# Kernel optimization log

Measured on AMD Instinct MI355X. Metric: run time of the kernel, lower is better.

The kernel has to match this reference:

```python
import jax, jax.numpy as jnp
import numpy as np

B, T, XD, H, ZD, L = 1024, 100, 38, 500, 16, 3


def _gru(x, Wih, Whh, bih, bhh):
    # torch nn.GRU (batch_first), gate order r,z,n. x: [B,T,D] -> [B,T,H]
    Hh = Whh.shape[1]
    xW = jnp.einsum('btd,gd->btg', x, Wih) + bih  # precompute input proj [B,T,3H]
    def step(h, xw_t):
        hW = h @ Whh.T + bhh
        r = jax.nn.sigmoid(xw_t[:, :Hh] + hW[:, :Hh])
        zg = jax.nn.sigmoid(xw_t[:, Hh:2 * Hh] + hW[:, Hh:2 * Hh])
        n = jnp.tanh(xw_t[:, 2 * Hh:] + r * hW[:, 2 * Hh:])
        h_new = (1.0 - zg) * n + zg * h
        return h_new, h_new
    h0 = jnp.zeros((x.shape[0], Hh), x.dtype)
    _, hs = jax.lax.scan(step, h0, jnp.swapaxes(xW, 0, 1))
    return jnp.swapaxes(hs, 0, 1)


def _u_hat(u, w):
    # invertibility-constrained u for planar flow
    wu = jnp.dot(w, u)
    m = -1.0 + jax.nn.softplus(wu)
    return u + (m - wu) * w / (jnp.sum(w * w) + 1e-6)


def setup_inputs() -> dict:
    key = jax.random.key(0)
    ks = jax.random.split(key, 24)
    def lin_init(k, shape, fan_in):
        bound = 1.0 / np.sqrt(fan_in)
        return jax.random.uniform(k, shape, jnp.float32, -bound, bound)
    inp = {}
    inp['x'] = jax.random.normal(ks[0], (B, T, XD), jnp.float32)
    inp['eps'] = jax.random.normal(ks[1], (B, T, ZD), jnp.float32)
    # q_rnn GRU
    inp['Wih_q'] = lin_init(ks[2], (3 * H, XD), H)
    inp['Whh_q'] = lin_init(ks[3], (3 * H, H), H)
    inp['bih_q'] = lin_init(ks[4], (3 * H,), H)
    inp['bhh_q'] = lin_init(ks[5], (3 * H,), H)
    # q_mean / q_std linears on [h_t, z_prev]
    inp['Wqm'] = lin_init(ks[6], (ZD, H + ZD), H + ZD)
    inp['bqm'] = lin_init(ks[7], (ZD,), H + ZD)
    inp['Wqs'] = lin_init(ks[8], (ZD, H + ZD), H + ZD)
    inp['bqs'] = lin_init(ks[9], (ZD,), H + ZD)
    # p_rnn GRU
    inp['Wih_p'] = lin_init(ks[10], (3 * H, ZD), H)
    inp['Whh_p'] = lin_init(ks[11], (3 * H, H), H)
    inp['bih_p'] = lin_init(ks[12], (3 * H,), H)
    inp['bhh_p'] = lin_init(ks[13], (3 * H,), H)
    # p_mean / p_std linears
    inp['Wpm'] = lin_init(ks[14], (XD, H), H)
    inp['bpm'] = lin_init(ks[15], (XD,), H)
    inp['Wps'] = lin_init(ks[16], (XD, H), H)
    inp['bps'] = lin_init(ks[17], (XD,), H)
    # planar flow params (torch.randn init)
    inp['fu'] = jax.random.normal(ks[18], (L, ZD), jnp.float32)
    inp['fw'] = jax.random.normal(ks[19], (L, ZD), jnp.float32)
    inp['fb'] = jax.random.normal(ks[20], (L,), jnp.float32)
    return inp


def reference(x, eps, Wih_q, Whh_q, bih_q, bhh_q, Wqm, bqm, Wqs, bqs,
              Wih_p, Whh_p, bih_p, bhh_p, Wpm, bpm, Wps, bps, fu, fw, fb):
    q_out = _gru(x, Wih_q, Whh_q, bih_q, bhh_q)  # [B,T,H]
    u_hats = jax.vmap(_u_hat)(fu, fw)            # [L,ZD], data-independent

    def step(carry, inp_t):
        z_prev, ld_sum = carry
        h_t, eps_t = inp_t
        comb = jnp.concatenate([h_t, z_prev], axis=1)          # [B,H+ZD]
        mu = comb @ Wqm.T + bqm
        std = jax.nn.softplus(comb @ Wqs.T + bqs) + 1e-4
        zk = mu + eps_t * std
        for k in range(L):  # small fixed number of flows
            w = fw[k]; uh = u_hats[k]
            hh = jnp.tanh(zk @ w + fb[k])[:, None]             # [B,1]
            zk = zk + uh[None, :] * hh
            psi = (1.0 - hh * hh) * w[None, :]                 # [B,ZD]
            det = 1.0 + psi @ uh                               # [B]
            ld_sum = ld_sum + jnp.log(jnp.abs(det) + 1e-6)[:, None]
        return (zk, ld_sum), (zk, mu, std)

    z0 = jnp.zeros((x.shape[0], ZD), x.dtype)
    ld0 = jnp.zeros((x.shape[0], 1), x.dtype)
    (_, log_det_sum), (z_seq, z0_mu, z0_std) = jax.lax.scan(
        step, (z0, ld0), (jnp.swapaxes(q_out, 0, 1), jnp.swapaxes(eps, 0, 1)))
    z_seq = jnp.swapaxes(z_seq, 0, 1)
    z0_mu = jnp.swapaxes(z0_mu, 0, 1)
    z0_std = jnp.swapaxes(z0_std, 0, 1)

    p_out = _gru(z_seq, Wih_p, Whh_p, bih_p, bhh_p)            # [B,T,H]
    recon_mu = p_out @ Wpm.T + bpm
    recon_std = jax.nn.softplus(p_out @ Wps.T + bps) + 1e-4
    return recon_mu, recon_std, z_seq, z0_mu, z0_std, log_det_sum
```

## Files before the change

### kernel.cpp

```cpp
#include <hip/hip_runtime.h>
#include <cmath>


#define B_  1024
#define T_  100
#define XD_ 38
#define H_  500
#define ZD_ 16
#define L_  3
#define NPHASE (T_ + 3)

typedef short bf16x8 __attribute__((ext_vector_type(8)));
typedef float f32x4  __attribute__((ext_vector_type(4)));
typedef unsigned short ushort;

#define HS ((size_t)B_ * 512)
#define ZS ((size_t)B_ * 32)

#define MFMA16(a, b, c) __builtin_amdgcn_mfma_f32_16x16x32_bf16((a), (b), (c), 0, 0, 0)

static __device__ __forceinline__ ushort f2bf(float f) {
    union { float f; unsigned u; } v; v.f = f;
    return (ushort)((v.u + 0x7FFF + ((v.u >> 16) & 1)) >> 16);
}
static __device__ __forceinline__ float sigf(float x) { return 1.0f / (1.0f + __expf(-x)); }
static __device__ __forceinline__ float tanh_(float x) {
    float e = __expf(2.0f * x);
    return 1.0f - 2.0f / (e + 1.0f);
}
static __device__ __forceinline__ float softplus_(float x) {
    return fmaxf(x, 0.0f) + log1pf(__expf(-fabsf(x)));
}
static __device__ __forceinline__ float grp16_sum(float v) {
    v += __shfl_xor(v, 1, 16);
    v += __shfl_xor(v, 2, 16);
    v += __shfl_xor(v, 4, 16);
    v += __shfl_xor(v, 8, 16);
    return v;
}

static __device__ __forceinline__ unsigned aload(const unsigned* p) {
    return __hip_atomic_load(p, __ATOMIC_RELAXED, __HIP_MEMORY_SCOPE_AGENT);
}
static __device__ __forceinline__ void astore(unsigned* p, unsigned v) {
    __hip_atomic_store(p, v, __ATOMIC_RELAXED, __HIP_MEMORY_SCOPE_AGENT);
}

struct OmniArgs {
    const float *x, *eps;
    const float *Wih_q, *Whh_q, *bih_q, *bhh_q;
    const float *Wqm, *bqm, *Wqs, *bqs;
    const float *Wih_p, *Whh_p, *bih_p, *bhh_p;
    const float *Wpm, *bpm, *Wps, *bps;
    const float *fu, *fw, *fb;
    ushort *hqbf, *hpbf, *zbf, *Wqg, *Wpg;
    unsigned *bar;
    float *o_rm, *o_rs, *o_z, *o_zm, *o_zs, *o_ld;
};

static __device__ __forceinline__ void arrive(unsigned* slots, int slot,
                                              unsigned tgt, int tid) {
    asm volatile("s_waitcnt vmcnt(0)" ::: "memory");
    __syncthreads();
    if (tid == 0) astore(slots + slot * 32, tgt);
}
static __device__ __forceinline__ void waitall(unsigned* slots, unsigned tgt,
                                               int tid) {
    if (tid < 64) {
        const unsigned* sp = slots + (tid & 31) * 32;
        for (;;) {
            bool ok = aload(sp) >= tgt;
            if (__all(ok)) break;
            __builtin_amdgcn_s_sleep(1);
        }
    }
    __syncthreads();
    asm volatile("buffer_inv" ::: "memory");
}

__global__ __launch_bounds__(512)
void omni_persist(OmniArgs A)
{
    __shared__ ushort lds[55296] __attribute__((aligned(16)));
    __shared__ int sh_gc[2];

    const int tid = threadIdx.x;

    if (tid == 0) {
        unsigned xcd;
        asm volatile("s_getreg_b32 %0, hwreg(HW_REG_XCC_ID)" : "=s"(xcd));
        xcd &= 7u;
        unsigned s = __hip_atomic_fetch_add(A.bar + xcd * 2048 + 1152, 1u,
                                            __ATOMIC_RELAXED, __HIP_MEMORY_SCOPE_AGENT);
        sh_gc[0] = (int)xcd;
        sh_gc[1] = (int)(s & 31u);
    }
    __syncthreads();
    const int grp = sh_gc[0];
    const int qc  = sh_gc[1];
    unsigned* slots = A.bar + grp * 2048;

    const bool isRC = (qc < 5);
    const bool isFL = (qc >= 24);
    const int  flowIdx = qc - 24;
    const int  fw2 = flowIdx >> 1;
    const int  fmt = flowIdx & 1;
    const int  m0 = grp * 128;

    const int gtid = tid & 255;
    const bool isQg = (tid < 256);
    const int w2   = gtid >> 6;
    const int lane = tid & 63;
    const int ln   = lane & 15, qd = lane >> 4;

    const bool fwave = isQg && isFL && (w2 == fw2);

    ushort* Whl = lds + (isQg ? 0 : 24960);
    ushort* Wil = lds + (isQg ? 49920 : 53376);

    ushort* WqgG = A.Wqg + (size_t)grp * (32 * 544);
    ushort* WpgG = A.Wpg + (size_t)grp * (128 * 512);

    const int rA0 = m0 + w2*32 + ln;
    const int rA1 = rA0 + 16;
    const int rAf = fmt ? rA1 : rA0;

    {
        const float* WhhSrc = isQg ? A.Whh_q : A.Whh_p;
        for (int idx = gtid; idx < 3*16*512; idx += 256) {
            int k = idx & 511, n = (idx >> 9) & 15, g = idx >> 13;
            int col = qc*16 + n;
            float v = (k < H_ && col < H_) ? WhhSrc[(size_t)(g*H_ + col)*H_ + k] : 0.f;
            Whl[(g*16 + n)*520 + k] = f2bf(v);
        }
        if (isQg) {
            for (int idx = gtid; idx < 3*16*64; idx += 256) {
                int k = idx & 63, n = (idx >> 6) & 15, g = idx >> 10;
                int col = qc*16 + n;
                float v = (k < XD_ && col < H_) ? A.Wih_q[(size_t)(g*H_+col)*XD_ + k] : 0.f;
                Wil[(g*16 + n)*72 + k] = f2bf(v);
            }
            if (qc == 31) {
                for (int idx = gtid; idx < 32*544; idx += 256) {
                    int n = idx / 544, k = idx - n*544;
                    const float* src = (n < 16) ? (A.Wqm + n*(H_+ZD_))
                                                : (A.Wqs + (n-16)*(H_+ZD_));
                    float v = 0.f;
                    if (k < H_) v = src[k];
                    else if (k >= 512 && k < 512 + ZD_) v = src[H_ + (k - 512)];
                    WqgG[idx] = f2bf(v);
                }
            }
        } else {
            for (int idx = gtid; idx < 3*16*32; idx += 256) {
                int k = idx & 31, n = (idx >> 5) & 15, g = idx >> 9;
                int col = qc*16 + n;
                float v = (k < ZD_ && col < H_) ? A.Wih_p[(size_t)(g*H_+col)*ZD_ + k] : 0.f;
                Wil[(g*16 + n)*40 + k] = f2bf(v);
            }
            if (isRC) {
                for (int idx = gtid; idx < 16*512; idx += 256) {
                    int k = idx & 511, n = idx >> 9;
                    int col = qc*16 + n;
                    float v = 0.f;
                    if (k < H_) {
                        if (col < XD_)        v = A.Wpm[(size_t)col*H_ + k];
                        else if (col < 2*XD_) v = A.Wps[(size_t)(col - XD_)*H_ + k];
                    }
                    WpgG[(size_t)(qc*16 + n)*512 + k] = f2bf(v);
                }
            }
        }
    }

    const int colg = qc*16 + ln;
    float bR = 0.f, bZ = 0.f, bNx = 0.f, bNh = 0.f;
    {
        const float* bi = isQg ? A.bih_q : A.bih_p;
        const float* bh = isQg ? A.bhh_q : A.bhh_p;
        if (colg < H_) {
            bR  = bi[colg] + bh[colg];
            bZ  = bi[H_ + colg] + bh[H_ + colg];
            bNx = bi[2*H_ + colg];
            bNh = bh[2*H_ + colg];
        }
    }
    const int colr = qc*16 + ln;
    float brc = 0.f;
    if (isRC && !isQg) {
        if (colr < XD_) brc = A.bpm[colr];
        else if (colr < 2*XD_) brc = A.bps[colr - XD_];
    }

    float uhv[3], wvv[3], fbv[3], bqm_r = 0.f, bqs_r = 0.f;
    if (isFL) {
        bqm_r = A.bqm[ln]; bqs_r = A.bqs[ln];
        #pragma unroll
        for (int k = 0; k < 3; ++k) {
            float w_ = A.fw[k*ZD_ + ln], u_ = A.fu[k*ZD_ + ln];
            float wu = grp16_sum(w_*u_), ww = grp16_sum(w_*w_);
            uhv[k] = u_ + (-1.f + softplus_(wu) - wu) * w_ / (ww + 1e-6f);
            wvv[k] = w_; fbv[k] = A.fb[k];
        }
    }

    float hold[8];
    #pragma unroll
    for (int r = 0; r < 8; ++r) hold[r] = 0.f;
    float ldacc[4] = {0.f, 0.f, 0.f, 0.f};

    __syncthreads();

    for (int i = 0; i < NPHASE; ++i) {
        const int t = i, j = i - 1, u = i - 2, v = i - 3;
        const bool do_q = (t < T_);
        const bool do_f = fwave && (j >= 0) && (j < T_);
        const bool do_p = (u >= 0) && (u < T_);
        const bool do_r = isRC && (v >= 0) && (v < T_);

        const ushort* AgQ = A.hqbf + (size_t)((i-1) & 1) * HS;
        const ushort* AgP = A.hpbf + (size_t)((i-1) & 1) * HS;
        const ushort* ZgP = A.zbf  + (size_t)(u & 1) * ZS;

        f32x4 aR0[2], aR1[2], aNh[2], aNx[2], aC[2], aMf, aSf;
        #pragma unroll
        for (int mt = 0; mt < 2; ++mt) {
            aR0[mt] = f32x4{0.f,0.f,0.f,0.f}; aR1[mt] = f32x4{0.f,0.f,0.f,0.f};
            aNh[mt] = f32x4{0.f,0.f,0.f,0.f}; aNx[mt] = f32x4{0.f,0.f,0.f,0.f};
            aC[mt]  = f32x4{0.f,0.f,0.f,0.f};
        }
        aMf = f32x4{0.f,0.f,0.f,0.f}; aSf = f32x4{0.f,0.f,0.f,0.f};

        if (isQg) {
            if ((do_q && i > 0) || do_f) {
                #pragma unroll 4
                for (int kt = 0; kt < 16; ++kt) {
                    bf16x8 af0 = *(const bf16x8*)(AgQ + (size_t)rA0*512 + kt*32 + qd*8);
                    bf16x8 af1 = *(const bf16x8*)(AgQ + (size_t)rA1*512 + kt*32 + qd*8);
                    if (do_q) {
                        const ushort* wb = Whl + (size_t)ln*520 + kt*32 + qd*8;
                        bf16x8 b0 = *(const bf16x8*)(wb);
                        bf16x8 b1 = *(const bf16x8*)(wb + 16*520);
                        bf16x8 b2 = *(const bf16x8*)(wb + 32*520);
                        aR0[0] = MFMA16(af0, b0, aR0[0]);  aR0[1] = MFMA16(af1, b0, aR0[1]);
                        aR1[0] = MFMA16(af0, b1, aR1[0]);  aR1[1] = MFMA16(af1, b1, aR1[1]);
                        aNh[0] = MFMA16(af0, b2, aNh[0]);  aNh[1] = MFMA16(af1, b2, aNh[1]);
                    }
                    if (do_f) {
                        bf16x8 bM = *(const bf16x8*)(WqgG + (size_t)ln*544 + kt*32 + qd*8);
                        bf16x8 bS = *(const bf16x8*)(WqgG + (size_t)(16+ln)*544 + kt*32 + qd*8);
                        bf16x8 afx = fmt ? af1 : af0;
                        aMf = MFMA16(afx, bM, aMf);
                        aSf = MFMA16(afx, bS, aSf);
                    }
                }
            }
            if (do_q) {
                #pragma unroll
                for (int xt = 0; xt < 2; ++xt) {
                    bf16x8 af[2];
                    #pragma unroll
                    for (int mt = 0; mt < 2; ++mt) {
                        int row = (mt == 0) ? rA0 : rA1;
                        const float* xs = A.x + ((size_t)row*T_ + t)*XD_;
                        int d0 = xt*32 + qd*8;
                        unsigned pk[4];
                        #pragma unroll
                        for (int ii = 0; ii < 4; ++ii) {
                            int d = d0 + ii*2;
                            float v0 = 0.f, v1 = 0.f;
                            if (d + 1 < XD_) { float2 f = *(const float2*)(xs + d); v0 = f.x; v1 = f.y; }
                            else if (d < XD_) v0 = xs[d];
                            pk[ii] = (unsigned)f2bf(v0) | ((unsigned)f2bf(v1) << 16);
                        }
                        uint4 pa = make_uint4(pk[0], pk[1], pk[2], pk[3]);
                        af[mt] = *(bf16x8*)&pa;
                    }
                    const ushort* wb = Wil + (size_t)ln*72 + xt*32 + qd*8;
                    bf16x8 b0 = *(const bf16x8*)(wb);
                    bf16x8 b1 = *(const bf16x8*)(wb + 16*72);
                    bf16x8 b2 = *(const bf16x8*)(wb + 32*72);
                    aR0[0] = MFMA16(af[0], b0, aR0[0]);  aR0[1] = MFMA16(af[1], b0, aR0[1]);
                    aR1[0] = MFMA16(af[0], b1, aR1[0]);  aR1[1] = MFMA16(af[1], b1, aR1[1]);
                    aNx[0] = MFMA16(af[0], b2, aNx[0]);  aNx[1] = MFMA16(af[1], b2, aNx[1]);
                }
            }
        } else {
            if ((do_p && u > 0) || do_r) {
                #pragma unroll 4
                for (int kt = 0; kt < 16; ++kt) {
                    bf16x8 af0 = *(const bf16x8*)(AgP + (size_t)rA0*512 + kt*32 + qd*8);
                    bf16x8 af1 = *(const bf16x8*)(AgP + (size_t)rA1*512 + kt*32 + qd*8);
                    if (do_p) {
                        const ushort* wb = Whl + (size_t)ln*520 + kt*32 + qd*8;
                        bf16x8 b0 = *(const bf16x8*)(wb);
                        bf16x8 b1 = *(const bf16x8*)(wb + 16*520);
                        bf16x8 b2 = *(const bf16x8*)(wb + 32*520);
                        aR0[0] = MFMA16(af0, b0, aR0[0]);  aR0[1] = MFMA16(af1, b0, aR0[1]);
                        aR1[0] = MFMA16(af0, b1, aR1[0]);  aR1[1] = MFMA16(af1, b1, aR1[1]);
                        aNh[0] = MFMA16(af0, b2, aNh[0]);  aNh[1] = MFMA16(af1, b2, aNh[1]);
                    }
                    if (do_r) {
                        bf16x8 bC = *(const bf16x8*)(WpgG + (size_t)(qc*16+ln)*512 + kt*32 + qd*8);
                        aC[0] = MFMA16(af0, bC, aC[0]);  aC[1] = MFMA16(af1, bC, aC[1]);
                    }
                }
            }
            if (do_p) {
                bf16x8 af0 = *(const bf16x8*)(ZgP + (size_t)rA0*32 + qd*8);
                bf16x8 af1 = *(const bf16x8*)(ZgP + (size_t)rA1*32 + qd*8);
                const ushort* wb = Wil + (size_t)ln*40 + qd*8;
                bf16x8 b0 = *(const bf16x8*)(wb);
                bf16x8 b1 = *(const bf16x8*)(wb + 16*40);
                bf16x8 b2 = *(const bf16x8*)(wb + 32*40);
                aR0[0] = MFMA16(af0, b0, aR0[0]);  aR0[1] = MFMA16(af1, b0, aR0[1]);
                aR1[0] = MFMA16(af0, b1, aR1[0]);  aR1[1] = MFMA16(af1, b1, aR1[1]);
                aNx[0] = MFMA16(af0, b2, aNx[0]);  aNx[1] = MFMA16(af1, b2, aNx[1]);
            }
        }

        if (isQg && do_q) {
            ushort* Hb = A.hqbf + (size_t)(i & 1) * HS;
            #pragma unroll
            for (int mt = 0; mt < 2; ++mt)
                #pragma unroll
                for (int r = 0; r < 4; ++r) {
                    int row = m0 + w2*32 + mt*16 + qd*4 + r;
                    float rg = sigf(aR0[mt][r] + bR);
                    float zg = sigf(aR1[mt][r] + bZ);
                    float ng = tanh_(aNx[mt][r] + bNx + rg*(aNh[mt][r] + bNh));
                    float hn = (1.f - zg)*ng + zg*hold[mt*4 + r];
                    if (colg >= H_) hn = 0.f;
                    hold[mt*4 + r] = hn;
                    Hb[(size_t)row*512 + colg] = f2bf(hn);
                }
        }
        if (!isQg && do_p) {
            ushort* Hb = A.hpbf + (size_t)(i & 1) * HS;
            #pragma unroll
            for (int mt = 0; mt < 2; ++mt)
                #pragma unroll
                for (int r = 0; r < 4; ++r) {
                    int row = m0 + w2*32 + mt*16 + qd*4 + r;
                    float rg = sigf(aR0[mt][r] + bR);
                    float zg = sigf(aR1[mt][r] + bZ);
                    float ng = tanh_(aNx[mt][r] + bNx + rg*(aNh[mt][r] + bNh));
                    float hn = (1.f - zg)*ng + zg*hold[mt*4 + r];
                    if (colg >= H_) hn = 0.f;
                    hold[mt*4 + r] = hn;
                    Hb[(size_t)row*512 + colg] = f2bf(hn);
                }
        }

        float mu4[4], sd4[4], zk4[4];
        if (do_f) {
            if (j >= 1) {
                const ushort* zp = A.zbf + (size_t)((j-1) & 1) * ZS;
                bf16x8 bMz = *(const bf16x8*)(WqgG + (size_t)ln*544 + 512 + qd*8);
                bf16x8 bSz = *(const bf16x8*)(WqgG + (size_t)(16+ln)*544 + 512 + qd*8);
                bf16x8 az  = *(const bf16x8*)(zp + (size_t)rAf*32 + qd*8);
                aMf = MFMA16(az, bMz, aMf);
                aSf = MFMA16(az, bSz, aSf);
            }
            ushort* Zo = A.zbf + (size_t)(j & 1) * ZS;
            #pragma unroll
            for (int r = 0; r < 4; ++r) {
                int row = m0 + flowIdx*16 + qd*4 + r;
                float mu = aMf[r] + bqm_r;
                float sd = softplus_(aSf[r] + bqs_r) + 1e-4f;
                float ep = A.eps[((size_t)row*T_ + j)*ZD_ + ln];
                float zk = mu + ep*sd;
                mu4[r] = mu; sd4[r] = sd;
                float lsum = 0.f;
                #pragma unroll
                for (int k = 0; k < 3; ++k) {
                    float th = tanh_(grp16_sum(zk*wvv[k]) + fbv[k]);
                    zk = fmaf(uhv[k], th, zk);
                    float det = 1.f + grp16_sum((1.f - th*th)*wvv[k]*uhv[k]);
                    lsum += logf(fabsf(det) + 1e-6f);
                }
                zk4[r] = zk; ldacc[r] += lsum;
                Zo[(size_t)row*32 + ln]      = f2bf(zk);
                Zo[(size_t)row*32 + 16 + ln] = 0;
            }
        }

        arrive(slots, qc, (unsigned)(i + 1), tid);

        if (do_f) {
            #pragma unroll
            for (int r = 0; r < 4; ++r) {
                int row = m0 + flowIdx*16 + qd*4 + r;
                size_t oi = ((size_t)row*T_ + j)*ZD_ + ln;
                A.o_zm[oi] = mu4[r];
                A.o_zs[oi] = sd4[r];
                A.o_z[oi]  = zk4[r];
                if (j == T_ - 1 && ln == 0) A.o_ld[row] = ldacc[r];
            }
        }
        if (!isQg && do_r) {
            #pragma unroll
            for (int mt = 0; mt < 2; ++mt)
                #pragma unroll
                for (int r = 0; r < 4; ++r) {
                    int row = m0 + w2*32 + mt*16 + qd*4 + r;
                    size_t ob = ((size_t)row*T_ + v)*XD_;
                    float a = aC[mt][r];
                    if (colr < XD_)        A.o_rm[ob + colr] = a + brc;
                    else if (colr < 2*XD_) A.o_rs[ob + (colr - XD_)] =
                                               softplus_(a + brc) + 1e-4f;
                }
        }

        if (i < NPHASE - 1)
            waitall(slots, (unsigned)(i + 1), tid);
    }
}

extern "C" void kernel_launch(void* const* d_in, const int* in_sizes, int n_in,
                              void* d_out, int out_size, void* d_ws, size_t ws_size,
                              hipStream_t stream)
{
    (void)in_sizes; (void)n_in; (void)out_size; (void)ws_size;
    float* out = (float*)d_out;

    char* p = (char*)d_ws;
    auto alloc = [&](size_t bytes) { void* r = p; p += (bytes + 255) & ~(size_t)255; return r; };
    const size_t HSb = (size_t)1024 * 512 * sizeof(ushort);
    ushort* hqbf = (ushort*)alloc(2 * HSb);
    ushort* hpbf = (ushort*)alloc(2 * HSb);
    ushort* zbf  = (ushort*)alloc(2 * (size_t)1024 * 32 * sizeof(ushort));
    ushort* Wqg  = (ushort*)alloc((size_t)8 * 32 * 544 * sizeof(ushort));
    ushort* Wpg  = (ushort*)alloc((size_t)8 * 128 * 512 * sizeof(ushort));
    unsigned* bar = (unsigned*)alloc((size_t)8 * 2048 * sizeof(unsigned));

    hipMemsetAsync(bar, 0, (size_t)8 * 2048 * sizeof(unsigned), stream);

    OmniArgs a;
    a.x     = (const float*)d_in[0];
    a.eps   = (const float*)d_in[1];
    a.Wih_q = (const float*)d_in[2];
    a.Whh_q = (const float*)d_in[3];
    a.bih_q = (const float*)d_in[4];
    a.bhh_q = (const float*)d_in[5];
    a.Wqm   = (const float*)d_in[6];
    a.bqm   = (const float*)d_in[7];
    a.Wqs   = (const float*)d_in[8];
    a.bqs   = (const float*)d_in[9];
    a.Wih_p = (const float*)d_in[10];
    a.Whh_p = (const float*)d_in[11];
    a.bih_p = (const float*)d_in[12];
    a.bhh_p = (const float*)d_in[13];
    a.Wpm   = (const float*)d_in[14];
    a.bpm   = (const float*)d_in[15];
    a.Wps   = (const float*)d_in[16];
    a.bps   = (const float*)d_in[17];
    a.fu    = (const float*)d_in[18];
    a.fw    = (const float*)d_in[19];
    a.fb    = (const float*)d_in[20];
    a.hqbf = hqbf; a.hpbf = hpbf; a.zbf = zbf; a.Wqg = Wqg; a.Wpg = Wpg; a.bar = bar;
    a.o_rm = out;
    a.o_rs = out + 3891200;
    a.o_z  = out + 7782400;
    a.o_zm = out + 9420800;
    a.o_zs = out + 11059200;
    a.o_ld = out + 12697600;

    void* kargs[] = { &a };
    hipError_t err = hipLaunchCooperativeKernel((void*)omni_persist, dim3(256), dim3(512),
                                                kargs, 0, stream);
    if (err != hipSuccess) {
        (void)hipGetLastError();
        hipLaunchKernelGGL(omni_persist, dim3(256), dim3(512), 0, stream, a);
    }
}
```

Before: 1.656 ms.

## Cache Whh fragments in registers and pre-convert x to bf16 in prologue

Holds the first ten k-tiles of the r/z recurrent weight fragments in registers for the whole time loop, so fewer LDS loads are issued per step. Converts x to a padded bf16 buffer in a prologue, adding an extra grid barrier, so the per-step input projection becomes two vector loads instead of scalar float loads and conversions. Barrier targets shift by one and the zero padding of z is written only in the first steps. Also fully unrolls the k loops. The main risk is register pressure and lower occupancy from the cached fragments.

Measured after the change: 2.243 ms. 1.35x slower.

```diff
diff --git a/kernel.cpp b/kernel.cpp
--- a/kernel.cpp
+++ b/kernel.cpp
@@ -9,6 +9,7 @@
 #define ZD_ 16
 #define L_  3
 #define NPHASE (T_ + 3)
+#define NCACHE 10
 
 typedef short bf16x8 __attribute__((ext_vector_type(8)));
 typedef float f32x4  __attribute__((ext_vector_type(4)));
@@ -53,7 +54,7 @@
     const float *Wih_p, *Whh_p, *bih_p, *bhh_p;
     const float *Wpm, *bpm, *Wps, *bps;
     const float *fu, *fw, *fb;
-    ushort *hqbf, *hpbf, *zbf, *Wqg, *Wpg;
+    ushort *hqbf, *hpbf, *zbf, *Wqg, *Wpg, *xbf;
     unsigned *bar;
     float *o_rm, *o_rs, *o_z, *o_zm, *o_zs, *o_ld;
 };
@@ -171,6 +172,13 @@
                 }
             }
         }
+        for (int idx = qc*512 + tid; idx < 128*T_*64; idx += 32*512) {
+            int row = idx / (T_*64);
+            int rem = idx - row*(T_*64);
+            int tt = rem >> 6, k = rem & 63;
+            float v = (k < XD_) ? A.x[((size_t)(m0+row)*T_ + tt)*XD_ + k] : 0.f;
+            A.xbf[((size_t)(m0+row)*T_ + tt)*64 + k] = f2bf(v);
+        }
     }
 
     const int colg = qc*16 + ln;
@@ -211,6 +219,17 @@
 
     __syncthreads();
 
+    bf16x8 cb0[NCACHE], cb1[NCACHE];
+    #pragma unroll
+    for (int kt = 0; kt < NCACHE; ++kt) {
+        const ushort* wb = Whl + (size_t)ln*520 + kt*32 + qd*8;
+        cb0[kt] = *(const bf16x8*)(wb);
+        cb1[kt] = *(const bf16x8*)(wb + 16*520);
+    }
+
+    arrive(slots, qc, 1u, tid);
+    waitall(slots, 1u, tid);
+
     for (int i = 0; i < NPHASE; ++i) {
         const int t = i, j = i - 1, u = i - 2, v = i - 3;
         const bool do_q = (t < T_);
@@ -233,14 +252,18 @@
 
         if (isQg) {
             if ((do_q && i > 0) || do_f) {
-                #pragma unroll 4
+                #pragma unroll
                 for (int kt = 0; kt < 16; ++kt) {
                     bf16x8 af0 = *(const bf16x8*)(AgQ + (size_t)rA0*512 + kt*32 + qd*8);
                     bf16x8 af1 = *(const bf16x8*)(AgQ + (size_t)rA1*512 + kt*32 + qd*8);
                     if (do_q) {
                         const ushort* wb = Whl + (size_t)ln*520 + kt*32 + qd*8;
-                        bf16x8 b0 = *(const bf16x8*)(wb);
-                        bf16x8 b1 = *(const bf16x8*)(wb + 16*520);
+                        bf16x8 b0, b1;
+                        if (kt < NCACHE) { b0 = cb0[kt]; b1 = cb1[kt]; }
+                        else {
+                            b0 = *(const bf16x8*)(wb);
+                            b1 = *(const bf16x8*)(wb + 16*520);
+                        }
                         bf16x8 b2 = *(const bf16x8*)(wb + 32*520);
                         aR0[0] = MFMA16(af0, b0, aR0[0]);  aR0[1] = MFMA16(af1, b0, aR0[1]);
                         aR1[0] = MFMA16(af0, b1, aR1[0]);  aR1[1] = MFMA16(af1, b1, aR1[1]);
@@ -258,43 +281,31 @@
             if (do_q) {
                 #pragma unroll
                 for (int xt = 0; xt < 2; ++xt) {
-                    bf16x8 af[2];
-                    #pragma unroll
-                    for (int mt = 0; mt < 2; ++mt) {
-                        int row = (mt == 0) ? rA0 : rA1;
-                        const float* xs = A.x + ((size_t)row*T_ + t)*XD_;
-                        int d0 = xt*32 + qd*8;
-                        unsigned pk[4];
-                        #pragma unroll
-                        for (int ii = 0; ii < 4; ++ii) {
-                            int d = d0 + ii*2;
-                            float v0 = 0.f, v1 = 0.f;
-                            if (d + 1 < XD_) { float2 f = *(const float2*)(xs + d); v0 = f.x; v1 = f.y; }
-                            else if (d < XD_) v0 = xs[d];
-                            pk[ii] = (unsigned)f2bf(v0) | ((unsigned)f2bf(v1) << 16);
-                        }
-                        uint4 pa = make_uint4(pk[0], pk[1], pk[2], pk[3]);
-                        af[mt] = *(bf16x8*)&pa;
-                    }
+                    bf16x8 af0 = *(const bf16x8*)(A.xbf + ((size_t)rA0*T_ + t)*64 + xt*32 + qd*8);
+                    bf16x8 af1 = *(const bf16x8*)(A.xbf + ((size_t)rA1*T_ + t)*64 + xt*32 + qd*8);
                     const ushort* wb = Wil + (size_t)ln*72 + xt*32 + qd*8;
                     bf16x8 b0 = *(const bf16x8*)(wb);
                     bf16x8 b1 = *(const bf16x8*)(wb + 16*72);
                     bf16x8 b2 = *(const bf16x8*)(wb + 32*72);
-                    aR0[0] = MFMA16(af[0], b0, aR0[0]);  aR0[1] = MFMA16(af[1], b0, aR0[1]);
-                    aR1[0] = MFMA16(af[0], b1, aR1[0]);  aR1[1] = MFMA16(af[1], b1, aR1[1]);
-                    aNx[0] = MFMA16(af[0], b2, aNx[0]);  aNx[1] = MFMA16(af[1], b2, aNx[1]);
+                    aR0[0] = MFMA16(af0, b0, aR0[0]);  aR0[1] = MFMA16(af1, b0, aR0[1]);
+                    aR1[0] = MFMA16(af0, b1, aR1[0]);  aR1[1] = MFMA16(af1, b1, aR1[1]);
+                    aNx[0] = MFMA16(af0, b2, aNx[0]);  aNx[1] = MFMA16(af1, b2, aNx[1]);
                 }
             }
         } else {
             if ((do_p && u > 0) || do_r) {
-                #pragma unroll 4
+                #pragma unroll
                 for (int kt = 0; kt < 16; ++kt) {
                     bf16x8 af0 = *(const bf16x8*)(AgP + (size_t)rA0*512 + kt*32 + qd*8);
                     bf16x8 af1 = *(const bf16x8*)(AgP + (size_t)rA1*512 + kt*32 + qd*8);
                     if (do_p) {
                         const ushort* wb = Whl + (size_t)ln*520 + kt*32 + qd*8;
-                        bf16x8 b0 = *(const bf16x8*)(wb);
-                        bf16x8 b1 = *(const bf16x8*)(wb + 16*520);
+                        bf16x8 b0, b1;
+                        if (kt < NCACHE) { b0 = cb0[kt]; b1 = cb1[kt]; }
+                        else {
+                            b0 = *(const bf16x8*)(wb);
+                            b1 = *(const bf16x8*)(wb + 16*520);
+                        }
                         bf16x8 b2 = *(const bf16x8*)(wb + 32*520);
                         aR0[0] = MFMA16(af0, b0, aR0[0]);  aR0[1] = MFMA16(af1, b0, aR0[1]);
                         aR1[0] = MFMA16(af0, b1, aR1[0]);  aR1[1] = MFMA16(af1, b1, aR1[1]);
@@ -380,12 +391,12 @@
                     lsum += logf(fabsf(det) + 1e-6f);
                 }
                 zk4[r] = zk; ldacc[r] += lsum;
-                Zo[(size_t)row*32 + ln]      = f2bf(zk);
-                Zo[(size_t)row*32 + 16 + ln] = 0;
-            }
-        }
-
-        arrive(slots, qc, (unsigned)(i + 1), tid);
+                Zo[(size_t)row*32 + ln] = f2bf(zk);
+                if (j < 2) Zo[(size_t)row*32 + 16 + ln] = 0;
+            }
+        }
+
+        arrive(slots, qc, (unsigned)(i + 2), tid);
 
         if (do_f) {
             #pragma unroll
@@ -413,7 +424,7 @@
         }
 
         if (i < NPHASE - 1)
-            waitall(slots, (unsigned)(i + 1), tid);
+            waitall(slots, (unsigned)(i + 2), tid);
     }
 }
 
@@ -432,6 +443,7 @@
     ushort* zbf  = (ushort*)alloc(2 * (size_t)1024 * 32 * sizeof(ushort));
     ushort* Wqg  = (ushort*)alloc((size_t)8 * 32 * 544 * sizeof(ushort));
     ushort* Wpg  = (ushort*)alloc((size_t)8 * 128 * 512 * sizeof(ushort));
+    ushort* xbf  = (ushort*)alloc((size_t)1024 * 100 * 64 * sizeof(ushort));
     unsigned* bar = (unsigned*)alloc((size_t)8 * 2048 * sizeof(unsigned));
 
     hipMemsetAsync(bar, 0, (size_t)8 * 2048 * sizeof(unsigned), stream);
@@ -458,7 +470,8 @@
     a.fu    = (const float*)d_in[18];
     a.fw    = (const float*)d_in[19];
     a.fb    = (const float*)d_in[20];
-    a.hqbf = hqbf; a.hpbf = hpbf; a.zbf = zbf; a.Wqg = Wqg; a.Wpg = Wpg; a.bar = bar;
+    a.hqbf = hqbf; a.hpbf = hpbf; a.zbf = zbf; a.Wqg = Wqg; a.Wpg = Wpg;
+    a.xbf = xbf; a.bar = bar;
     a.o_rm = out;
     a.o_rs = out + 3891200;
     a.o_z  = out + 7782400;
```

## Split grid barrier into separate q/p half-block barriers with LDS flag handoff

Applied to the files above, without the earlier changes.

Replaces the block-wide __syncthreads plus a single group barrier with separate barrier slot arrays for the q-GRU and p-GRU halves of each block. Each half signals through LDS flags among its own waves and polls only the slots it depends on, with the q half allowed to run up to two phases ahead of the p half. The z buffer ring grows from 2 to 4 slots to allow that slack, and the zero padding of z is written only in the first phases. The aim is to cut barrier latency and decouple the two recurrences. In exchange, correctness now depends on the spin-wait handshake on volatile LDS flags being ordered correctly, and on the extra buffering being deep enough for the allowed lag.

Result: slower. 1.979 ms (+19.5%).

```diff
diff --git a/kernel.cpp b/kernel.cpp
--- a/kernel.cpp
+++ b/kernel.cpp
@@ -58,23 +58,36 @@
     float *o_rm, *o_rs, *o_z, *o_zm, *o_zs, *o_ld;
 };
 
-static __device__ __forceinline__ void arrive(unsigned* slots, int slot,
-                                              unsigned tgt, int tid) {
+static __device__ __forceinline__ void parr(unsigned* mySlots,
+                                            volatile unsigned* sfl,
+                                            int w2, int lane, int qc,
+                                            unsigned tgt) {
     asm volatile("s_waitcnt vmcnt(0)" ::: "memory");
-    __syncthreads();
-    if (tid == 0) astore(slots + slot * 32, tgt);
-}
-static __device__ __forceinline__ void waitall(unsigned* slots, unsigned tgt,
-                                               int tid) {
-    if (tid < 64) {
-        const unsigned* sp = slots + (tid & 31) * 32;
+    if (w2 != 0) {
+        if (lane == 0) sfl[w2] = tgt;
+    } else {
+        while (sfl[1] < tgt || sfl[2] < tgt || sfl[3] < tgt)
+            __builtin_amdgcn_s_sleep(1);
+        if (lane == 0) astore(mySlots + qc * 32, tgt);
+    }
+}
+static __device__ __forceinline__ void pwait(unsigned* mySlots, unsigned* othSlots,
+                                             volatile unsigned* sfl,
+                                             int w2, int lane,
+                                             unsigned tgt, unsigned othNeed) {
+    if (w2 == 0) {
+        const unsigned* sp = (lane < 32) ? (mySlots + (lane & 31) * 32)
+                                         : (othSlots + (lane & 31) * 32);
+        const unsigned need = (lane < 32) ? tgt : othNeed;
         for (;;) {
-            bool ok = aload(sp) >= tgt;
+            bool ok = aload(sp) >= need;
             if (__all(ok)) break;
             __builtin_amdgcn_s_sleep(1);
         }
-    }
-    __syncthreads();
+        if (lane == 0) sfl[4] = tgt;
+    } else {
+        while (sfl[4] < tgt) __builtin_amdgcn_s_sleep(1);
+    }
     asm volatile("buffer_inv" ::: "memory");
 }
 
@@ -82,6 +95,7 @@
 void omni_persist(OmniArgs A)
 {
     __shared__ ushort lds[55296] __attribute__((aligned(16)));
+    __shared__ unsigned sflags[16];
     __shared__ int sh_gc[2];
 
     const int tid = threadIdx.x;
@@ -90,15 +104,17 @@
         unsigned xcd;
         asm volatile("s_getreg_b32 %0, hwreg(HW_REG_XCC_ID)" : "=s"(xcd));
         xcd &= 7u;
-        unsigned s = __hip_atomic_fetch_add(A.bar + xcd * 2048 + 1152, 1u,
+        unsigned s = __hip_atomic_fetch_add(A.bar + xcd * 4096 + 2080, 1u,
                                             __ATOMIC_RELAXED, __HIP_MEMORY_SCOPE_AGENT);
         sh_gc[0] = (int)xcd;
         sh_gc[1] = (int)(s & 31u);
     }
+    if (tid < 16) sflags[tid] = 0;
     __syncthreads();
     const int grp = sh_gc[0];
     const int qc  = sh_gc[1];
-    unsigned* slots = A.bar + grp * 2048;
+    unsigned* qslots = A.bar + grp * 4096;
+    unsigned* pslots = qslots + 1024;
 
     const bool isRC = (qc < 5);
     const bool isFL = (qc >= 24);
@@ -120,6 +136,10 @@
 
     ushort* WqgG = A.Wqg + (size_t)grp * (32 * 544);
     ushort* WpgG = A.Wpg + (size_t)grp * (128 * 512);
+
+    unsigned* mySlots  = isQg ? qslots : pslots;
+    unsigned* othSlots = isQg ? pslots : qslots;
+    volatile unsigned* sfl = (volatile unsigned*)(isQg ? sflags : sflags + 8);
 
     const int rA0 = m0 + w2*32 + ln;
     const int rA1 = rA0 + 16;
@@ -220,7 +240,7 @@
 
         const ushort* AgQ = A.hqbf + (size_t)((i-1) & 1) * HS;
         const ushort* AgP = A.hpbf + (size_t)((i-1) & 1) * HS;
-        const ushort* ZgP = A.zbf  + (size_t)(u & 1) * ZS;
+        const ushort* ZgP = A.zbf  + (size_t)(u & 3) * ZS;
 
         f32x4 aR0[2], aR1[2], aNh[2], aNx[2], aC[2], aMf, aSf;
         #pragma unroll
@@ -355,14 +375,14 @@
         float mu4[4], sd4[4], zk4[4];
         if (do_f) {
             if (j >= 1) {
-                const ushort* zp = A.zbf + (size_t)((j-1) & 1) * ZS;
+                const ushort* zp = A.zbf + (size_t)((j-1) & 3) * ZS;
                 bf16x8 bMz = *(const bf16x8*)(WqgG + (size_t)ln*544 + 512 + qd*8);
                 bf16x8 bSz = *(const bf16x8*)(WqgG + (size_t)(16+ln)*544 + 512 + qd*8);
                 bf16x8 az  = *(const bf16x8*)(zp + (size_t)rAf*32 + qd*8);
                 aMf = MFMA16(az, bMz, aMf);
                 aSf = MFMA16(az, bSz, aSf);
             }
-            ushort* Zo = A.zbf + (size_t)(j & 1) * ZS;
+            ushort* Zo = A.zbf + (size_t)(j & 3) * ZS;
             #pragma unroll
             for (int r = 0; r < 4; ++r) {
                 int row = m0 + flowIdx*16 + qd*4 + r;
@@ -380,12 +400,15 @@
                     lsum += logf(fabsf(det) + 1e-6f);
                 }
                 zk4[r] = zk; ldacc[r] += lsum;
-                Zo[(size_t)row*32 + ln]      = f2bf(zk);
-                Zo[(size_t)row*32 + 16 + ln] = 0;
-            }
-        }
-
-        arrive(slots, qc, (unsigned)(i + 1), tid);
+                Zo[(size_t)row*32 + ln] = f2bf(zk);
+                if (j < 4) Zo[(size_t)row*32 + 16 + ln] = 0;
+            }
+        }
+
+        const unsigned tgt = (unsigned)(i + 1);
+        const unsigned othNeed = isQg ? (tgt >= 3 ? tgt - 2 : 0) : tgt;
+
+        parr(mySlots, sfl, w2, lane, qc, tgt);
 
         if (do_f) {
             #pragma unroll
@@ -413,7 +436,7 @@
         }
 
         if (i < NPHASE - 1)
-            waitall(slots, (unsigned)(i + 1), tid);
+            pwait(mySlots, othSlots, sfl, w2, lane, tgt, othNeed);
     }
 }
 
@@ -429,12 +452,12 @@
     const size_t HSb = (size_t)1024 * 512 * sizeof(ushort);
     ushort* hqbf = (ushort*)alloc(2 * HSb);
     ushort* hpbf = (ushort*)alloc(2 * HSb);
-    ushort* zbf  = (ushort*)alloc(2 * (size_t)1024 * 32 * sizeof(ushort));
+    ushort* zbf  = (ushort*)alloc(4 * (size_t)1024 * 32 * sizeof(ushort));
     ushort* Wqg  = (ushort*)alloc((size_t)8 * 32 * 544 * sizeof(ushort));
     ushort* Wpg  = (ushort*)alloc((size_t)8 * 128 * 512 * sizeof(ushort));
-    unsigned* bar = (unsigned*)alloc((size_t)8 * 2048 * sizeof(unsigned));
-
-    hipMemsetAsync(bar, 0, (size_t)8 * 2048 * sizeof(unsigned), stream);
+    unsigned* bar = (unsigned*)alloc((size_t)8 * 4096 * sizeof(unsigned));
+
+    hipMemsetAsync(bar, 0, (size_t)8 * 4096 * sizeof(unsigned), stream);
 
     OmniArgs a;
     a.x     = (const float*)d_in[0];
```
